# Kernel optimization log

Hardware: AMD Instinct MI355X
Metric: run time of the kernel (lower is better)

Reference implementation:

```python
import jax, jax.numpy as jnp
import numpy as np

L, KV, H, D, DM, F, V = 6, 1, 4, 256, 1152, 6912, 65536
HIST, T = 4095, 1
EPS = 1e-6


def setup_inputs():
    key = jax.random.key(0)
    ks = jax.random.split(key, 24)
    n = lambda k, s, sc=0.02: jax.random.normal(k, s, dtype=jnp.float32) * sc
    sf = D ** -0.25  # head_dim^-0.25 baked into q/k norm weights as in the source
    return {
        "input_ids": jax.random.randint(ks[0], (1, T), 0, V, dtype=jnp.int32),
        "attn_flag": 0,  # decode step: additive causal mask zeroed, as in the repo
        "key_cache": n(ks[1], (L, KV, D, HIST), 0.5),
        "value_cache": n(ks[2], (L, KV, HIST, D), 0.5),
        "embed_table": jax.random.randint(ks[3], (V, DM), 0, 256, dtype=jnp.int32),
        "embed_scale": jax.random.uniform(ks[4], (V, 1), minval=1e-4, maxval=1e-2, dtype=jnp.float32),
        "embed_zp": -jax.random.uniform(ks[5], (V, 1), minval=0.0, maxval=0.5, dtype=jnp.float32),
        "w_in_ln": 1.0 + n(ks[6], (L, DM)),
        "w_q_norm": (1.0 + n(ks[7], (L, D))) * sf,
        "w_k_norm": (1.0 + n(ks[8], (L, D))) * sf,
        "Wq": n(ks[9], (L, DM, H * D)),
        "Wk": n(ks[10], (L, DM, KV * D)),
        "Wv": n(ks[11], (L, DM, KV * D)),
        "Wo": n(ks[12], (L, H * D, DM)),
        "w_post_attn_ln": 1.0 + n(ks[13], (L, DM)),
        "w_pre_ffn_ln": 1.0 + n(ks[14], (L, DM)),
        "w_post_ffn_ln": 1.0 + n(ks[15], (L, DM)),
        "Wg": n(ks[16], (L, DM, F)),
        "Wu": n(ks[17], (L, DM, F)),
        "Wd": n(ks[18], (L, F, DM)),
        "w_final_norm": 1.0 + n(ks[19], (DM,)),
        "W_lm": n(ks[20], (DM, V)),
        "is_sliding": (jnp.arange(L) % 6) != 5,  # 5 local : 1 global pattern
    }


def _rms(x, w):
    return w * x / jnp.sqrt(jnp.mean(x * x, axis=-1, keepdims=True) + EPS)


def _rot_half(x, axis):
    x1, x2 = jnp.split(x, 2, axis=axis)
    return jnp.concatenate([-x2, x1], axis=axis)


def _rope(base, hist, S, d):
    pos = jnp.arange(hist, S, dtype=jnp.float32)[:, None]
    theta = base ** (-(jnp.arange(0, d, 2, dtype=jnp.float32) / d))
    ang = pos * theta
    c = jnp.concatenate([jnp.cos(ang)] * 2, axis=-1).astype(jnp.float16).astype(jnp.float32)
    s = jnp.concatenate([jnp.sin(ang)] * 2, axis=-1).astype(jnp.float16).astype(jnp.float32)
    return c, s  # (T, D), half-precision roundtrip mimics the .half() tables


def reference(input_ids, attn_flag, key_cache, value_cache, embed_table, embed_scale,
              embed_zp, w_in_ln, w_q_norm, w_k_norm, Wq, Wk, Wv, Wo, w_post_attn_ln,
              w_pre_ffn_ln, w_post_ffn_ln, Wg, Wu, Wd, w_final_norm, W_lm, is_sliding):
    Lc, KVc, Dd, hist = key_cache.shape
    Tq = input_ids.shape[1]
    S = hist + Tq
    Hh = Wq.shape[-1] // Dd
    G = Hh // KVc
    cos_g, sin_g = _rope(10000.0, hist, S, Dd)    # assigned to 'global' exactly as in source
    cos_l, sin_l = _rope(1000000.0, hist, S, Dd)  # assigned to 'local'
    mask = (jnp.arange(S)[None, :] > jnp.arange(Tq)[:, None]).astype(jnp.float32) * (-128.0 * float(attn_flag))  # (T,S)
    # int8-dequant embedding lookup: uint8 codes * per-row scale + per-row zero point
    h = embed_table[input_ids].astype(jnp.float32) * embed_scale[input_ids] + embed_zp[input_ids]  # (1,T,DM)

    def body(h, xs):
        ck, cv, slide, w_in, w_qn, w_kn, wq, wk, wv, wo, w_pa, w_pf, w_pof, wg, wu, wd = xs
        cq = jnp.where(slide, cos_l, cos_g)
        sq = jnp.where(slide, sin_l, sin_g)
        ckk, skk = cq.T, sq.T  # (D,T) for keys
        resid = h
        hn = _rms(h, w_in)                                                  # (1,T,DM)
        q = _rms((hn @ wq).reshape(Tq, Hh, Dd), w_qn).transpose(1, 0, 2)    # (H,T,D)
        k = _rms((hn @ wk).reshape(Tq, KVc, Dd), w_kn).transpose(1, 2, 0)   # (KV,D,T)
        v = (hn @ wv).reshape(Tq, KVc, Dd).transpose(1, 0, 2)               # (KV,T,D)
        q = q * cq + _rot_half(q, -1) * sq
        k = k * ckk[None] + _rot_half(k, 1) * skk[None]
        kf = jnp.concatenate([ck, k], axis=-1)   # (KV,D,S) new key cache
        vf = jnp.concatenate([cv, v], axis=1)    # (KV,S,D) new value cache
        kr = jnp.repeat(kf, G, axis=0)           # GQA repeat -> (H,D,S)
        vr = jnp.repeat(vf, G, axis=0)           # (H,S,D)
        attn = jax.nn.softmax(jnp.einsum('htd,hds->hts', q, kr) + mask[None], axis=-1)
        ao = jnp.einsum('hts,hsd->htd', attn, vr).transpose(1, 0, 2).reshape(1, Tq, Hh * Dd) @ wo
        h = resid + _rms(ao, w_pa)
        resid = h
        x = _rms(h, w_pf)
        m = (jax.nn.gelu(x @ wg, approximate=True) * (x @ wu)) @ wd
        h = resid + _rms(m, w_pof)
        return h, (kf, vf)

    h, (keys, values) = jax.lax.scan(
        body, h,
        (key_cache, value_cache, is_sliding, w_in_ln, w_q_norm, w_k_norm, Wq, Wk, Wv, Wo,
         w_post_attn_ln, w_pre_ffn_ln, w_post_ffn_ln, Wg, Wu, Wd))
    last = _rms(h[:, -1], w_final_norm)          # (1,DM)
    logits = last @ W_lm                          # (1,V)
    token = jnp.argmax(logits, axis=-1, keepdims=True).astype(jnp.int32)
    return keys, values, token
```

## Files before the change

kernel.cpp:

```cpp
#include <hip/hip_runtime.h>
#include <hip/hip_fp16.h>
#include <cmath>

#define LNUM 6
#define DM   1152
#define DHEAD 256
#define NH   4
#define FF   6912
#define VOC  65536
#define HIST 4095
#define SEQ  4096
#define EPSV 1e-6f

__device__ __forceinline__ float block_sum(float v, float* red4) {
#pragma unroll
    for (int off = 32; off; off >>= 1) v += __shfl_xor(v, off);
    int t = threadIdx.x;
    if ((t & 63) == 0) red4[t >> 6] = v;
    __syncthreads();
    float r = red4[0] + red4[1] + red4[2] + red4[3];
    __syncthreads();
    return r;
}

__global__ __launch_bounds__(256) void gk_copy(const float* __restrict__ kc,
                                               const float* __restrict__ vc,
                                               float* __restrict__ keys,
                                               float* __restrict__ vals) {
    int b = blockIdx.x;
    if (b < 24576) {
        int row = b >> 4;
        int s = ((b & 15) << 8) + threadIdx.x;
        if (s < HIST) keys[(size_t)row * SEQ + s] = kc[(size_t)row * HIST + s];
    } else {
        int r = (b - 24576) * 4 + (threadIdx.x >> 6);
        int d4 = threadIdx.x & 63;
        if (r < LNUM * HIST) {
            int l = r / HIST, sI = r - l * HIST;
            ((float4*)(vals + ((size_t)l * SEQ + sI) * DHEAD))[d4] =
                ((const float4*)(vc + (size_t)r * DHEAD))[d4];
        }
    }
}

__global__ __launch_bounds__(256) void gk_qkv(
    const float* __restrict__ Wq, const float* __restrict__ Wk, const float* __restrict__ Wv,
    const float* __restrict__ w_in, const float* __restrict__ w_pof_prev,
    const float* __restrict__ hprev, const float* __restrict__ dprev,
    const int* __restrict__ ids, const int* __restrict__ tbl,
    const float* __restrict__ escale, const float* __restrict__ ezp,
    float* __restrict__ hin_out, float* __restrict__ qkv_out, int has_prev) {
    __shared__ float xv[DM];
    __shared__ float red4[4];
    int t = threadIdx.x;
    if (has_prev) {
        float ss = 0.f;
        for (int i = t; i < DM; i += 256) { float d = dprev[i]; ss += d * d; }
        ss = block_sum(ss, red4);
        float inv = 1.f / sqrtf(ss / DM + EPSV);
        for (int i = t; i < DM; i += 256)
            xv[i] = hprev[i] + w_pof_prev[i] * dprev[i] * inv;
    } else {
        int tok = ids[0];
        float sc = escale[tok], z = ezp[tok];
        const int* row = tbl + (size_t)tok * DM;
        for (int i = t; i < DM; i += 256) xv[i] = (float)row[i] * sc + z;
    }
    __syncthreads();
    if (blockIdx.x == 0 && blockIdx.y == 0)
        for (int i = t; i < DM; i += 256) hin_out[i] = xv[i];
    float ss = 0.f;
    for (int i = t; i < DM; i += 256) { float v = xv[i]; ss += v * v; }
    ss = block_sum(ss, red4);
    float inv = 1.f / sqrtf(ss / DM + EPSV);
    for (int i = t; i < DM; i += 256) xv[i] = w_in[i] * xv[i] * inv;
    __syncthreads();

    int j = blockIdx.x * 256 + t;
    const float* W; int jj, ncol;
    if (j < 1024)      { W = Wq; jj = j;        ncol = 1024; }
    else if (j < 1280) { W = Wk; jj = j - 1024; ncol = 256; }
    else               { W = Wv; jj = j - 1280; ncol = 256; }
    int i0 = blockIdx.y * 36;
    float acc = 0.f;
#pragma unroll 4
    for (int ii = 0; ii < 36; ++ii)
        acc += xv[i0 + ii] * W[(size_t)(i0 + ii) * ncol + jj];
    atomicAdd(&qkv_out[j], acc);
}

__global__ __launch_bounds__(256) void gk_attn(
    const float* __restrict__ qkv, const float* __restrict__ w_qn,
    const float* __restrict__ w_kn, const int* __restrict__ attn_flag,
    float* __restrict__ keys_l, float* __restrict__ vals_l,
    float* __restrict__ po_part, float* __restrict__ sum_part, float rope_base) {
    __shared__ float lq[NH * DHEAD];
    __shared__ float lqf[NH * DHEAD];
    __shared__ float lkn[DHEAD];
    __shared__ float lkf[DHEAD];
    __shared__ float lv[DHEAD];
    __shared__ float lp[NH * 32];
    __shared__ float red4[4];
    int t = threadIdx.x;
    int s0 = blockIdx.x * 32;
    bool last = (blockIdx.x == gridDim.x - 1);

    int jm = t & 127;
    float theta = powf(rope_base, -(float)(2 * jm) / 256.f);
    float ang = 4095.f * theta;
    float c = __half2float(__float2half(cosf(ang)));
    float s = __half2float(__float2half(sinf(ang)));

    for (int h = 0; h < NH; ++h) lq[h * 256 + t] = qkv[h * 256 + t];
    lkn[t] = qkv[1024 + t];
    lv[t]  = qkv[1280 + t];
    __syncthreads();
    for (int h = 0; h < NH; ++h) {
        float v = lq[h * 256 + t];
        float ss = block_sum(v * v, red4);
        float inv = 1.f / sqrtf(ss / 256.f + EPSV);
        float qn = w_qn[t] * v * inv;
        lq[h * 256 + t] = qn;
        __syncthreads();
        float partner = (t < 128) ? -lq[h * 256 + t + 128] : lq[h * 256 + t - 128];
        lqf[h * 256 + t] = qn * c + partner * s;
    }
    {
        float v = lkn[t];
        float ss = block_sum(v * v, red4);
        float inv = 1.f / sqrtf(ss / 256.f + EPSV);
        float kn = w_kn[t] * v * inv;
        lkn[t] = kn;
        __syncthreads();
        float partner = (t < 128) ? -lkn[t + 128] : lkn[t - 128];
        lkf[t] = kn * c + partner * s;
    }
    __syncthreads();
    if (last) {
        keys_l[(size_t)t * SEQ + (SEQ - 1)] = lkf[t];
        vals_l[(size_t)(SEQ - 1) * DHEAD + t] = lv[t];
    }
    int sl = t & 31, dc = t >> 5;
    int sg = s0 + sl;
    bool self = last && (sl == 31);
    float a0 = 0, a1 = 0, a2 = 0, a3 = 0;
#pragma unroll 4
    for (int dd = 0; dd < 32; ++dd) {
        int d = dc * 32 + dd;
        float kv = self ? lkf[d] : keys_l[(size_t)d * SEQ + sg];
        a0 += lqf[0 * 256 + d] * kv;
        a1 += lqf[1 * 256 + d] * kv;
        a2 += lqf[2 * 256 + d] * kv;
        a3 += lqf[3 * 256 + d] * kv;
    }
    __syncthreads();
    lq[0 * 256 + t] = a0; lq[1 * 256 + t] = a1; lq[2 * 256 + t] = a2; lq[3 * 256 + t] = a3;
    __syncthreads();
    if (t < 32) {
        int af = attn_flag[0];
        float mk = (s0 + t > 0) ? -128.f * (float)af : 0.f;
        for (int h = 0; h < NH; ++h) {
            float sc_ = 0.f;
#pragma unroll
            for (int d8 = 0; d8 < 8; ++d8) sc_ += lq[h * 256 + d8 * 32 + t];
            lp[h * 32 + t] = expf(sc_ + mk);
        }
    }
    __syncthreads();
    if (t < NH) {
        float su = 0.f;
        for (int i = 0; i < 32; ++i) su += lp[t * 32 + i];
        sum_part[blockIdx.x * NH + t] = su;
    }
    float p0 = 0, p1 = 0, p2 = 0, p3 = 0;
#pragma unroll 4
    for (int ss_ = 0; ss_ < 32; ++ss_) {
        float v = (last && ss_ == 31) ? lv[t] : vals_l[(size_t)(s0 + ss_) * DHEAD + t];
        p0 += lp[0 * 32 + ss_] * v;
        p1 += lp[1 * 32 + ss_] * v;
        p2 += lp[2 * 32 + ss_] * v;
        p3 += lp[3 * 32 + ss_] * v;
    }
    float* po = po_part + (size_t)blockIdx.x * NH * DHEAD;
    po[0 * 256 + t] = p0; po[1 * 256 + t] = p1; po[2 * 256 + t] = p2; po[3 * 256 + t] = p3;
}

__global__ __launch_bounds__(256) void gk_wo(
    const float* __restrict__ po_part, const float* __restrict__ sum_part,
    const float* __restrict__ Wo_l, float* __restrict__ aproj) {
    __shared__ float x[64];
    __shared__ float hinv[NH];
    __shared__ float red4[4];
    int t = threadIdx.x;
    for (int h = 0; h < NH; ++h) {
        float v = (t < 128) ? sum_part[t * NH + h] : 0.f;
        float tot = block_sum(v, red4);
        if (t == 0) hinv[h] = 1.f / tot;
    }
    __syncthreads();
    int i0 = blockIdx.y * 64;
    if (t < 64) {
        float a = 0.f;
#pragma unroll 8
        for (int b = 0; b < 128; ++b) a += po_part[(size_t)b * 1024 + i0 + t];
        x[t] = a * hinv[(i0 + t) >> 8];
    }
    __syncthreads();
    int j = blockIdx.x * 256 + t;
    if (j < DM) {
        float acc = 0.f;
#pragma unroll 4
        for (int ii = 0; ii < 64; ++ii)
            acc += x[ii] * Wo_l[(size_t)(i0 + ii) * DM + j];
        atomicAdd(&aproj[j], acc);
    }
}

__global__ __launch_bounds__(256) void gk_gu(
    const float* __restrict__ Wg_l, const float* __restrict__ Wu_l,
    const float* __restrict__ w_pa, const float* __restrict__ w_pf,
    const float* __restrict__ hin, const float* __restrict__ aproj,
    float* __restrict__ hmid_out, float* __restrict__ gup) {
    __shared__ float xv[DM];
    __shared__ float red4[4];
    int t = threadIdx.x;
    float ss = 0.f;
    for (int i = t; i < DM; i += 256) { float a = aproj[i]; ss += a * a; }
    ss = block_sum(ss, red4);
    float inv = 1.f / sqrtf(ss / DM + EPSV);
    for (int i = t; i < DM; i += 256) xv[i] = hin[i] + w_pa[i] * aproj[i] * inv;
    __syncthreads();
    if (blockIdx.x == 0 && blockIdx.y == 0)
        for (int i = t; i < DM; i += 256) hmid_out[i] = xv[i];
    float s2 = 0.f;
    for (int i = t; i < DM; i += 256) { float v = xv[i]; s2 += v * v; }
    s2 = block_sum(s2, red4);
    float inv2 = 1.f / sqrtf(s2 / DM + EPSV);
    for (int i = t; i < DM; i += 256) xv[i] = w_pf[i] * xv[i] * inv2;
    __syncthreads();

    int j2 = blockIdx.x * 256 + t;
    const float2* W2; int jj2; float* dst;
    if (j2 < FF / 2) { W2 = (const float2*)Wg_l; jj2 = j2;
                       dst = gup + (size_t)blockIdx.y * 2 * FF + 2 * j2; }
    else             { W2 = (const float2*)Wu_l; jj2 = j2 - FF / 2;
                       dst = gup + (size_t)blockIdx.y * 2 * FF + FF + 2 * (j2 - FF / 2); }
    int i0 = blockIdx.y * 72;
    float ax = 0.f, ay = 0.f;
#pragma unroll 4
    for (int ii = 0; ii < 72; ++ii) {
        float xs = xv[i0 + ii];
        float2 w = W2[(size_t)(i0 + ii) * (FF / 2) + jj2];
        ax += xs * w.x; ay += xs * w.y;
    }
    dst[0] = ax; dst[1] = ay;
}

__global__ __launch_bounds__(256) void gk_wd(const float* __restrict__ gup,
                                             const float* __restrict__ Wd_l,
                                             float* __restrict__ dproj) {
    __shared__ float m[108];
    int t = threadIdx.x;
    int i0 = blockIdx.y * 108;
    if (t < 108) {
        float g = 0.f, u = 0.f;
#pragma unroll
        for (int p = 0; p < 16; ++p) {
            g += gup[(size_t)p * 2 * FF + i0 + t];
            u += gup[(size_t)p * 2 * FF + FF + i0 + t];
        }
        float gl = 0.5f * g * (1.f + tanhf(0.7978845608028654f * (g + 0.044715f * g * g * g)));
        m[t] = gl * u;
    }
    __syncthreads();
    int j = blockIdx.x * 256 + t;
    if (j < DM) {
        float acc = 0.f;
#pragma unroll 4
        for (int ii = 0; ii < 108; ++ii)
            acc += m[ii] * Wd_l[(size_t)(i0 + ii) * DM + j];
        atomicAdd(&dproj[j], acc);
    }
}

__global__ __launch_bounds__(256) void gk_logits(
    const float* __restrict__ W_lm, const float* __restrict__ w_pof5,
    const float* __restrict__ w_fin, const float* __restrict__ hmid5,
    const float* __restrict__ dproj5, float* __restrict__ lgp) {
    __shared__ float xv[DM];
    __shared__ float red4[4];
    int t = threadIdx.x;
    float ss = 0.f;
    for (int i = t; i < DM; i += 256) { float d = dproj5[i]; ss += d * d; }
    ss = block_sum(ss, red4);
    float inv = 1.f / sqrtf(ss / DM + EPSV);
    for (int i = t; i < DM; i += 256) xv[i] = hmid5[i] + w_pof5[i] * dproj5[i] * inv;
    __syncthreads();
    float s2 = 0.f;
    for (int i = t; i < DM; i += 256) { float v = xv[i]; s2 += v * v; }
    s2 = block_sum(s2, red4);
    float inv2 = 1.f / sqrtf(s2 / DM + EPSV);
    for (int i = t; i < DM; i += 256) xv[i] = w_fin[i] * xv[i] * inv2;
    __syncthreads();

    int j2 = blockIdx.x * 256 + t;
    int i0 = blockIdx.y * 192;
    const float2* W2 = (const float2*)W_lm;
    float ax = 0.f, ay = 0.f;
#pragma unroll 4
    for (int ii = 0; ii < 192; ++ii) {
        float xs = xv[i0 + ii];
        float2 w = W2[(size_t)(i0 + ii) * (VOC / 2) + j2];
        ax += xs * w.x; ay += xs * w.y;
    }
    float* dst = lgp + (size_t)blockIdx.y * VOC + 2 * j2;
    dst[0] = ax; dst[1] = ay;
}

__global__ __launch_bounds__(256) void gk_amax1(const float* __restrict__ lgp,
                                                float* __restrict__ pv, float* __restrict__ pi) {
    __shared__ float rv[256];
    __shared__ int ri[256];
    int t = threadIdx.x;
    int c1 = blockIdx.x * 512 + t, c2 = c1 + 256;
    float v1 = 0.f, v2 = 0.f;
#pragma unroll
    for (int p = 0; p < 6; ++p) {
        v1 += lgp[(size_t)p * VOC + c1];
        v2 += lgp[(size_t)p * VOC + c2];
    }
    float bv; int bi;
    if (v1 >= v2) { bv = v1; bi = c1; } else { bv = v2; bi = c2; }
    rv[t] = bv; ri[t] = bi; __syncthreads();
    for (int off = 128; off > 0; off >>= 1) {
        if (t < off) {
            float ov = rv[t + off]; int oi = ri[t + off];
            if (ov > rv[t] || (ov == rv[t] && oi < ri[t])) { rv[t] = ov; ri[t] = oi; }
        }
        __syncthreads();
    }
    if (t == 0) { pv[blockIdx.x] = rv[0]; pi[blockIdx.x] = (float)ri[0]; }
}

__global__ __launch_bounds__(128) void gk_amax2(const float* __restrict__ pv,
                                                const float* __restrict__ pi,
                                                float* __restrict__ tok_out) {
    __shared__ float rv[128];
    __shared__ int ri[128];
    int t = threadIdx.x;
    rv[t] = pv[t]; ri[t] = (int)pi[t]; __syncthreads();
    for (int off = 64; off > 0; off >>= 1) {
        if (t < off) {
            float ov = rv[t + off]; int oi = ri[t + off];
            if (ov > rv[t] || (ov == rv[t] && oi < ri[t])) { rv[t] = ov; ri[t] = oi; }
        }
        __syncthreads();
    }
    if (t == 0) tok_out[0] = (float)ri[0];
}

extern "C" void kernel_launch(void* const* d_in, const int* in_sizes, int n_in,
                              void* d_out, int out_size, void* d_ws, size_t ws_size,
                              hipStream_t stream) {
    const int*   input_ids   = (const int*)d_in[0];
    const int*   attn_flag   = (const int*)d_in[1];
    const float* key_cache   = (const float*)d_in[2];
    const float* value_cache = (const float*)d_in[3];
    const int*   embed_table = (const int*)d_in[4];
    const float* embed_scale = (const float*)d_in[5];
    const float* embed_zp    = (const float*)d_in[6];
    const float* w_in_ln     = (const float*)d_in[7];
    const float* w_q_norm    = (const float*)d_in[8];
    const float* w_k_norm    = (const float*)d_in[9];
    const float* Wq          = (const float*)d_in[10];
    const float* Wk          = (const float*)d_in[11];
    const float* Wv          = (const float*)d_in[12];
    const float* Wo          = (const float*)d_in[13];
    const float* w_pa        = (const float*)d_in[14];
    const float* w_pf        = (const float*)d_in[15];
    const float* w_pof       = (const float*)d_in[16];
    const float* Wg          = (const float*)d_in[17];
    const float* Wu          = (const float*)d_in[18];
    const float* Wd          = (const float*)d_in[19];
    const float* w_fin       = (const float*)d_in[20];
    const float* W_lm        = (const float*)d_in[21];

    float* keys = (float*)d_out;
    float* vals = keys + (size_t)LNUM * DHEAD * SEQ;
    float* tok_out = vals + (size_t)LNUM * SEQ * DHEAD;

    float* ws = (float*)d_ws;
    const size_t QKV_O = 0;
    const size_t AP_O  = QKV_O + (size_t)LNUM * 1536;
    const size_t DP_O  = AP_O + (size_t)LNUM * DM;
    const size_t ZEND  = DP_O + (size_t)LNUM * DM;
    const size_t POP_O = ZEND;
    const size_t SPS_O = POP_O + 128 * 1024;
    const size_t GUP_O = SPS_O + 128 * NH;
    const size_t LGP_O = GUP_O + (size_t)16 * 2 * FF;
    const size_t HIN_O = LGP_O + (size_t)6 * VOC;
    const size_t HM_O  = HIN_O + (size_t)LNUM * DM;
    const size_t AMV_O = HM_O + (size_t)LNUM * DM;
    const size_t AMI_O = AMV_O + 128;

    hipMemsetAsync(ws, 0, ZEND * sizeof(float), stream);
    gk_copy<<<24576 + 6144, 256, 0, stream>>>(key_cache, value_cache, keys, vals);

    for (int l = 0; l < LNUM; ++l) {
        float* QKVl = ws + QKV_O + (size_t)l * 1536;
        float* APl  = ws + AP_O + (size_t)l * DM;
        float* DPl  = ws + DP_O + (size_t)l * DM;
        float* HINl = ws + HIN_O + (size_t)l * DM;
        float* HMl  = ws + HM_O + (size_t)l * DM;
        float* keys_l = keys + (size_t)l * DHEAD * SEQ;
        float* vals_l = vals + (size_t)l * SEQ * DHEAD;

        gk_qkv<<<dim3(6, 32), 256, 0, stream>>>(
            Wq + (size_t)l * DM * 1024, Wk + (size_t)l * DM * 256,
            Wv + (size_t)l * DM * 256, w_in_ln + (size_t)l * DM,
            w_pof + (size_t)(l ? l - 1 : 0) * DM,
            (l ? ws + HM_O + (size_t)(l - 1) * DM : nullptr),
            (l ? ws + DP_O + (size_t)(l - 1) * DM : nullptr),
            input_ids, embed_table, embed_scale, embed_zp,
            HINl, QKVl, (l > 0) ? 1 : 0);

        gk_attn<<<128, 256, 0, stream>>>(
            QKVl, w_q_norm + (size_t)l * DHEAD, w_k_norm + (size_t)l * DHEAD,
            attn_flag, keys_l, vals_l, ws + POP_O, ws + SPS_O,
            ((l % 6) != 5) ? 1000000.0f : 10000.0f);

        gk_wo<<<dim3(5, 16), 256, 0, stream>>>(
            ws + POP_O, ws + SPS_O, Wo + (size_t)l * 1024 * DM, APl);

        gk_gu<<<dim3(27, 16), 256, 0, stream>>>(
            Wg + (size_t)l * DM * FF, Wu + (size_t)l * DM * FF,
            w_pa + (size_t)l * DM, w_pf + (size_t)l * DM, HINl, APl, HMl, ws + GUP_O);

        gk_wd<<<dim3(5, 64), 256, 0, stream>>>(ws + GUP_O, Wd + (size_t)l * FF * DM, DPl);
    }

    gk_logits<<<dim3(128, 6), 256, 0, stream>>>(
        W_lm, w_pof + (size_t)5 * DM, w_fin,
        ws + HM_O + (size_t)5 * DM, ws + DP_O + (size_t)5 * DM, ws + LGP_O);
    gk_amax1<<<128, 256, 0, stream>>>(ws + LGP_O, ws + AMV_O, ws + AMI_O);
    gk_amax2<<<1, 128, 0, stream>>>(ws + AMV_O, ws + AMI_O, tok_out);
}
```

Baseline: 596.0 us.

## Fuse per-layer decoder kernels into one persistent cooperative megakernel with grid syncs

Replaces the memset, cache copy and the five per-layer kernel launches with a single cooperative persistent kernel of 256 blocks that uses grid-wide syncs between stages. Work is redistributed into loops over work units, with new split-K tilings and in-block reductions before the atomics for Wo, gate/up and down projections. The goal is to remove launch overhead and inter-kernel gaps across roughly 30 launches. The risk is grid-sync cost, lower occupancy from 32KB of shared memory, and reduced parallelism on stages that now cover fewer units than before; a fallback multi-kernel path runs if the cooperative launch fails.

New measurement: 1.329 ms. 2.23x slower.

```diff
diff --git a/kernel.cpp b/kernel.cpp
--- a/kernel.cpp
+++ b/kernel.cpp
@@ -1,6 +1,9 @@
 #include <hip/hip_runtime.h>
 #include <hip/hip_fp16.h>
+#include <hip/hip_cooperative_groups.h>
 #include <cmath>
+
+namespace cg = cooperative_groups;
 
 #define LNUM 6
 #define DM   1152
@@ -11,8 +14,384 @@
 #define HIST 4095
 #define SEQ  4096
 #define EPSV 1e-6f
-
-__device__ __forceinline__ float block_sum(float v, float* red4) {
+#define NB   256
+
+#define QKV_O 0
+#define AP_O  9216
+#define DP_O  16128
+#define GU_O  23040
+#define ZEND  105984
+#define HIN_O 105984
+#define HM_O  112896
+#define POP_O 119808
+#define SPS_O 250880
+#define LGP_O 251392
+#define AMV_O 775680
+#define AMI_O 775936
+
+#define F_QKV_O 0
+#define F_AP_O  9216
+#define F_DP_O  16128
+#define F_ZEND  23040
+#define F_POP_O 23040
+#define F_SPS_O 154112
+#define F_GUP_O 154624
+#define F_LGP_O 375808
+#define F_HIN_O 769024
+#define F_HM_O  775936
+#define F_AMV_O 782848
+#define F_AMI_O 782976
+
+struct P {
+    const int* ids; const int* aflag;
+    const float* kc; const float* vc;
+    const int* tbl; const float* esc; const float* ezp;
+    const float* w_in; const float* w_qn; const float* w_kn;
+    const float* Wq; const float* Wk; const float* Wv; const float* Wo;
+    const float* w_pa; const float* w_pf; const float* w_pof;
+    const float* Wg; const float* Wu; const float* Wd;
+    const float* w_fin; const float* Wlm;
+    float* keys; float* vals; float* tok; float* ws;
+};
+
+__device__ __forceinline__ float bsum(float v, float* red4) {
+#pragma unroll
+    for (int off = 32; off; off >>= 1) v += __shfl_xor(v, off);
+    int t = threadIdx.x;
+    if ((t & 63) == 0) red4[t >> 6] = v;
+    __syncthreads();
+    float r = red4[0] + red4[1] + red4[2] + red4[3];
+    __syncthreads();
+    return r;
+}
+
+__global__ __launch_bounds__(256) void mega(P p) {
+    cg::grid_group gg = cg::this_grid();
+    __shared__ float sm[8192];
+    const int t = threadIdx.x, bid = blockIdx.x;
+    float* ws = p.ws;
+
+    {
+        for (int g = bid * 256 + t; g < ZEND; g += NB * 256) ws[g] = 0.f;
+        if (bid == 0) {
+            int tk = p.ids[0];
+            float sc = p.esc[tk], z = p.ezp[tk];
+            const int* row = p.tbl + (size_t)tk * DM;
+            for (int i = t; i < DM; i += 256) ws[HIN_O + i] = (float)row[i] * sc + z;
+        }
+        for (int rr = 0; rr < 6; ++rr) {
+            int row = bid * 6 + rr;
+            const float* src = p.kc + (size_t)row * HIST;
+            float* dst = p.keys + (size_t)row * SEQ;
+            for (int s = t; s < HIST; s += 256) dst[s] = src[s];
+        }
+        for (int rr = 0; rr < 24; ++rr) {
+            int r = bid * 96 + rr * 4 + (t >> 6);
+            if (r < LNUM * HIST) {
+                int l = r / HIST, sI = r - l * HIST;
+                ((float4*)(p.vals + ((size_t)l * SEQ + sI) * DHEAD))[t & 63] =
+                    ((const float4*)(p.vc + (size_t)r * DHEAD))[t & 63];
+            }
+        }
+    }
+    gg.sync();
+
+    for (int l = 0; l < LNUM; ++l) {
+        float* QKV = ws + QKV_O + l * 1536;
+        float* AP  = ws + AP_O + l * DM;
+        float* DP  = ws + DP_O + l * DM;
+        float* GU  = ws + GU_O + l * 13824;
+        float* HIN = ws + HIN_O + l * DM;
+        float* HM  = ws + HM_O + l * DM;
+        float* POP = ws + POP_O;
+        float* SPS = ws + SPS_O;
+        float* keys_l = p.keys + (size_t)l * DHEAD * SEQ;
+        float* vals_l = p.vals + (size_t)l * SEQ * DHEAD;
+
+        {
+            float* xv = sm; float* red4 = sm + 1280;
+            if (l == 0) {
+                for (int i = t; i < DM; i += 256) xv[i] = ws[HIN_O + i];
+                __syncthreads();
+            } else {
+                const float* hprev = ws + HM_O + (l - 1) * DM;
+                const float* dprev = ws + DP_O + (l - 1) * DM;
+                const float* wpof = p.w_pof + (l - 1) * DM;
+                float ss = 0.f;
+                for (int i = t; i < DM; i += 256) { float d = dprev[i]; ss += d * d; }
+                ss = bsum(ss, red4);
+                float inv = 1.f / sqrtf(ss / DM + EPSV);
+                for (int i = t; i < DM; i += 256)
+                    xv[i] = hprev[i] + wpof[i] * dprev[i] * inv;
+                __syncthreads();
+            }
+            if (bid == 0) for (int i = t; i < DM; i += 256) HIN[i] = xv[i];
+            float ss = 0.f;
+            for (int i = t; i < DM; i += 256) { float v = xv[i]; ss += v * v; }
+            ss = bsum(ss, red4);
+            float inv = 1.f / sqrtf(ss / DM + EPSV);
+            const float* w_in = p.w_in + l * DM;
+            for (int i = t; i < DM; i += 256) xv[i] = w_in[i] * xv[i] * inv;
+            __syncthreads();
+            for (int u = bid; u < 384; u += NB) {
+                int cgp = u % 6, kc = u / 6;
+                int j = cgp * 256 + t;
+                const float* W; int jj, ncol;
+                if (j < 1024)      { W = p.Wq + (size_t)l * DM * 1024; jj = j;        ncol = 1024; }
+                else if (j < 1280) { W = p.Wk + (size_t)l * DM * 256;  jj = j - 1024; ncol = 256; }
+                else               { W = p.Wv + (size_t)l * DM * 256;  jj = j - 1280; ncol = 256; }
+                int i0 = kc * 18;
+                float acc = 0.f;
+#pragma unroll
+                for (int ii = 0; ii < 18; ++ii)
+                    acc += xv[i0 + ii] * W[(size_t)(i0 + ii) * ncol + jj];
+                atomicAdd(&QKV[j], acc);
+            }
+        }
+        gg.sync();
+
+        if (bid < 128) {
+            float* lq = sm;
+            float* lqf = sm + 1024;
+            float* lkn = sm + 2048;
+            float* lkf = sm + 2304;
+            float* lv  = sm + 2560;
+            float* lp  = sm + 2816;
+            float* red4 = sm + 2944;
+            float* scred = sm + 3072;
+            float* pvred = sm + 4096;
+            int s0 = bid * 32;
+            bool lastb = (bid == 127);
+            float base = ((l % 6) != 5) ? 1000000.f : 10000.f;
+            int jm = t & 127;
+            float theta = powf(base, -(float)(2 * jm) / 256.f);
+            float ang = 4095.f * theta;
+            float c = __half2float(__float2half(cosf(ang)));
+            float s = __half2float(__float2half(sinf(ang)));
+            for (int h = 0; h < NH; ++h) lq[h * 256 + t] = QKV[h * 256 + t];
+            lkn[t] = QKV[1024 + t];
+            lv[t]  = QKV[1280 + t];
+            __syncthreads();
+            const float* wqn = p.w_qn + l * DHEAD;
+            const float* wkn = p.w_kn + l * DHEAD;
+            for (int h = 0; h < NH; ++h) {
+                float v = lq[h * 256 + t];
+                float ss = bsum(v * v, red4);
+                float inv = 1.f / sqrtf(ss / 256.f + EPSV);
+                float qn = wqn[t] * v * inv;
+                lq[h * 256 + t] = qn;
+                __syncthreads();
+                float partner = (t < 128) ? -lq[h * 256 + t + 128] : lq[h * 256 + t - 128];
+                lqf[h * 256 + t] = qn * c + partner * s;
+            }
+            {
+                float v = lkn[t];
+                float ss = bsum(v * v, red4);
+                float inv = 1.f / sqrtf(ss / 256.f + EPSV);
+                float kn = wkn[t] * v * inv;
+                lkn[t] = kn;
+                __syncthreads();
+                float partner = (t < 128) ? -lkn[t + 128] : lkn[t - 128];
+                lkf[t] = kn * c + partner * s;
+            }
+            __syncthreads();
+            if (lastb) {
+                keys_l[(size_t)t * SEQ + (SEQ - 1)] = lkf[t];
+                vals_l[(size_t)(SEQ - 1) * DHEAD + t] = lv[t];
+            }
+            int sl = t & 31, dc = t >> 5;
+            int sg = s0 + sl;
+            bool self = lastb && (sl == 31);
+            float a0 = 0, a1 = 0, a2 = 0, a3 = 0;
+#pragma unroll 4
+            for (int dd = 0; dd < 32; ++dd) {
+                int d = dc * 32 + dd;
+                float kv = self ? lkf[d] : keys_l[(size_t)d * SEQ + sg];
+                a0 += lqf[d] * kv; a1 += lqf[256 + d] * kv;
+                a2 += lqf[512 + d] * kv; a3 += lqf[768 + d] * kv;
+            }
+            scred[dc * 128 + sl]      = a0;
+            scred[dc * 128 + 32 + sl] = a1;
+            scred[dc * 128 + 64 + sl] = a2;
+            scred[dc * 128 + 96 + sl] = a3;
+            __syncthreads();
+            if (t < 32) {
+                int af = p.aflag[0];
+                float mk = (s0 + t > 0) ? -128.f * (float)af : 0.f;
+                for (int h = 0; h < NH; ++h) {
+                    float sc_ = 0.f;
+#pragma unroll
+                    for (int d8 = 0; d8 < 8; ++d8) sc_ += scred[d8 * 128 + h * 32 + t];
+                    lp[h * 32 + t] = expf(sc_ + mk);
+                }
+            }
+            __syncthreads();
+            if (t < NH) {
+                float su = 0.f;
+                for (int i = 0; i < 32; ++i) su += lp[t * 32 + i];
+                SPS[bid * NH + t] = su;
+            }
+            int d4 = t & 63, sr = t >> 6;
+            float4 ac0 = {0,0,0,0}, ac1 = {0,0,0,0}, ac2 = {0,0,0,0}, ac3 = {0,0,0,0};
+#pragma unroll
+            for (int ss_ = 0; ss_ < 8; ++ss_) {
+                int sI = sr * 8 + ss_;
+                float4 v;
+                if (lastb && sI == 31) v = ((float4*)lv)[d4];
+                else v = ((const float4*)(vals_l + (size_t)(s0 + sI) * DHEAD))[d4];
+                float p0 = lp[sI], p1 = lp[32 + sI], p2 = lp[64 + sI], p3 = lp[96 + sI];
+                ac0.x += p0 * v.x; ac0.y += p0 * v.y; ac0.z += p0 * v.z; ac0.w += p0 * v.w;
+                ac1.x += p1 * v.x; ac1.y += p1 * v.y; ac1.z += p1 * v.z; ac1.w += p1 * v.w;
+                ac2.x += p2 * v.x; ac2.y += p2 * v.y; ac2.z += p2 * v.z; ac2.w += p2 * v.w;
+                ac3.x += p3 * v.x; ac3.y += p3 * v.y; ac3.z += p3 * v.z; ac3.w += p3 * v.w;
+            }
+            ((float4*)(pvred + sr * 1024 + 0))[d4]   = ac0;
+            ((float4*)(pvred + sr * 1024 + 256))[d4] = ac1;
+            ((float4*)(pvred + sr * 1024 + 512))[d4] = ac2;
+            ((float4*)(pvred + sr * 1024 + 768))[d4] = ac3;
+            __syncthreads();
+            for (int o = t; o < 1024; o += 256) {
+                float v = pvred[o] + pvred[1024 + o] + pvred[2048 + o] + pvred[3072 + o];
+                POP[(size_t)bid * 1024 + o] = v;
+            }
+        }
+        gg.sync();
+
+        {
+            float* hinv = sm;
+            float* xred = sm + 8;
+            float* xl = sm + 272;
+            float* red4 = sm + 312;
+            float* wored = sm + 320;
+            for (int h = 0; h < NH; ++h) {
+                float v = (t < 128) ? SPS[t * NH + h] : 0.f;
+                float tot = bsum(v, red4);
+                if (t == 0) hinv[h] = 1.f / tot;
+            }
+            __syncthreads();
+            const float* Wo_l = p.Wo + (size_t)l * 1024 * DM;
+            for (int u = bid; u < 288; u += NB) {
+                __syncthreads();
+                int cgp = u % 9, kc = u / 9;
+                int i0 = kc * 32;
+                { int li = t & 31, bg = t >> 5;
+                  float a = 0.f;
+                  for (int b = bg * 16; b < bg * 16 + 16; ++b) a += POP[(size_t)b * 1024 + i0 + li];
+                  xred[bg * 32 + li] = a; }
+                __syncthreads();
+                if (t < 32) {
+                    float a = 0.f;
+#pragma unroll
+                    for (int bg = 0; bg < 8; ++bg) a += xred[bg * 32 + t];
+                    xl[t] = a * hinv[(i0 + t) >> 8];
+                }
+                __syncthreads();
+                int col = cgp * 128 + (t & 127);
+                int kh = t >> 7;
+                float acc = 0.f;
+#pragma unroll
+                for (int r = 0; r < 16; ++r) {
+                    int li = kh * 16 + r;
+                    acc += xl[li] * Wo_l[(size_t)(i0 + li) * DM + col];
+                }
+                wored[t] = acc;
+                __syncthreads();
+                if (t < 128) atomicAdd(&AP[cgp * 128 + t], wored[t] + wored[128 + t]);
+            }
+        }
+        gg.sync();
+
+        {
+            float* xv = sm; float* red4 = sm + 1152; float* gred = sm + 1184;
+            float ss = 0.f;
+            for (int i = t; i < DM; i += 256) { float a = AP[i]; ss += a * a; }
+            ss = bsum(ss, red4);
+            float inv = 1.f / sqrtf(ss / DM + EPSV);
+            const float* wpa = p.w_pa + l * DM;
+            for (int i = t; i < DM; i += 256) xv[i] = HIN[i] + wpa[i] * AP[i] * inv;
+            __syncthreads();
+            if (bid == 0) for (int i = t; i < DM; i += 256) HM[i] = xv[i];
+            float s2 = 0.f;
+            for (int i = t; i < DM; i += 256) { float v = xv[i]; s2 += v * v; }
+            s2 = bsum(s2, red4);
+            float inv2 = 1.f / sqrtf(s2 / DM + EPSV);
+            const float* wpf = p.w_pf + l * DM;
+            for (int i = t; i < DM; i += 256) xv[i] = wpf[i] * xv[i] * inv2;
+            __syncthreads();
+            for (int u = bid; u < 486; u += NB) {
+                __syncthreads();
+                int cgi = u % 54, kc = u / 54;
+                bool isU = cgi >= 27;
+                int cgp = isU ? cgi - 27 : cgi;
+                const float* W = (isU ? p.Wu : p.Wg) + (size_t)l * DM * FF;
+                int f4c = t & 63, ks = t >> 6;
+                int colf = cgp * 64 + f4c;
+                int i0 = kc * 128 + ks * 32;
+                float4 acc = {0,0,0,0};
+#pragma unroll 4
+                for (int r = 0; r < 32; ++r) {
+                    float xs = xv[i0 + r];
+                    float4 w = ((const float4*)(W + (size_t)(i0 + r) * FF))[colf];
+                    acc.x += xs * w.x; acc.y += xs * w.y; acc.z += xs * w.z; acc.w += xs * w.w;
+                }
+                ((float4*)gred)[ks * 64 + f4c] = acc;
+                __syncthreads();
+                if (ks == 0) {
+                    float4 r0 = ((float4*)gred)[f4c],       r1 = ((float4*)gred)[64 + f4c],
+                           r2 = ((float4*)gred)[128 + f4c], r3 = ((float4*)gred)[192 + f4c];
+                    float* dst = GU + (isU ? FF : 0) + colf * 4;
+                    atomicAdd(dst + 0, r0.x + r1.x + r2.x + r3.x);
+                    atomicAdd(dst + 1, r0.y + r1.y + r2.y + r3.y);
+                    atomicAdd(dst + 2, r0.z + r1.z + r2.z + r3.z);
+                    atomicAdd(dst + 3, r0.w + r1.w + r2.w + r3.w);
+                }
+            }
+        }
+        gg.sync();
+
+        {
+            float* m = sm;
+            float* wred = sm + 128;
+            const float* Wd_l = p.Wd + (size_t)l * FF * DM;
+            for (int u = bid; u < 486; u += NB) {
+                __syncthreads();
+                int cgp = u % 9, kc = u / 9;
+                int i0 = kc * 128;
+                if (t < 128) {
+                    float g = GU[i0 + t], uu = GU[FF + i0 + t];
+                    float gl = 0.5f * g * (1.f + tanhf(0.7978845608028654f * (g + 0.044715f * g * g * g)));
+                    m[t] = gl * uu;
+                }
+                __syncthreads();
+                int f4c = t & 31, ks = t >> 5;
+                float4 acc = {0,0,0,0};
+#pragma unroll 4
+                for (int r = 0; r < 16; ++r) {
+                    int li = ks * 16 + r;
+                    float xs = m[li];
+                    float4 w = ((const float4*)(Wd_l + (size_t)(i0 + li) * DM))[cgp * 32 + f4c];
+                    acc.x += xs * w.x; acc.y += xs * w.y; acc.z += xs * w.z; acc.w += xs * w.w;
+                }
+                ((float4*)wred)[ks * 32 + f4c] = acc;
+                __syncthreads();
+                if (ks == 0) {
+                    float sx = 0, sy = 0, sz = 0, sw = 0;
+#pragma unroll
+                    for (int k2 = 0; k2 < 8; ++k2) {
+                        float4 r = ((float4*)wred)[k2 * 32 + f4c];
+                        sx += r.x; sy += r.y; sz += r.z; sw += r.w;
+                    }
+                    float* dst = DP + cgp * 128 + f4c * 4;
+                    atomicAdd(dst + 0, sx); atomicAdd(dst + 1, sy);
+                    atomicAdd(dst + 2, sz); atomicAdd(dst + 3, sw);
+                }
+            }
+        }
+        gg.sync();
+    }
+}
+
+__device__ __forceinline__ float block_sum256(float v, float* red4) {
 #pragma unroll
     for (int off = 32; off; off >>= 1) v += __shfl_xor(v, off);
     int t = threadIdx.x;
@@ -56,7 +435,7 @@
     if (has_prev) {
         float ss = 0.f;
         for (int i = t; i < DM; i += 256) { float d = dprev[i]; ss += d * d; }
-        ss = block_sum(ss, red4);
+        ss = block_sum256(ss, red4);
         float inv = 1.f / sqrtf(ss / DM + EPSV);
         for (int i = t; i < DM; i += 256)
             xv[i] = hprev[i] + w_pof_prev[i] * dprev[i] * inv;
@@ -71,7 +450,7 @@
         for (int i = t; i < DM; i += 256) hin_out[i] = xv[i];
     float ss = 0.f;
     for (int i = t; i < DM; i += 256) { float v = xv[i]; ss += v * v; }
-    ss = block_sum(ss, red4);
+    ss = block_sum256(ss, red4);
     float inv = 1.f / sqrtf(ss / DM + EPSV);
     for (int i = t; i < DM; i += 256) xv[i] = w_in[i] * xv[i] * inv;
     __syncthreads();
@@ -117,7 +496,7 @@
     __syncthreads();
     for (int h = 0; h < NH; ++h) {
         float v = lq[h * 256 + t];
-        float ss = block_sum(v * v, red4);
+        float ss = block_sum256(v * v, red4);
         float inv = 1.f / sqrtf(ss / 256.f + EPSV);
         float qn = w_qn[t] * v * inv;
         lq[h * 256 + t] = qn;
@@ -127,7 +506,7 @@
     }
     {
         float v = lkn[t];
-        float ss = block_sum(v * v, red4);
+        float ss = block_sum256(v * v, red4);
         float inv = 1.f / sqrtf(ss / 256.f + EPSV);
         float kn = w_kn[t] * v * inv;
         lkn[t] = kn;
@@ -194,7 +573,7 @@
     int t = threadIdx.x;
     for (int h = 0; h < NH; ++h) {
         float v = (t < 128) ? sum_part[t * NH + h] : 0.f;
-        float tot = block_sum(v, red4);
+        float tot = block_sum256(v, red4);
         if (t == 0) hinv[h] = 1.f / tot;
     }
     __syncthreads();
@@ -226,7 +605,7 @@
     int t = threadIdx.x;
     float ss = 0.f;
     for (int i = t; i < DM; i += 256) { float a = aproj[i]; ss += a * a; }
-    ss = block_sum(ss, red4);
+    ss = block_sum256(ss, red4);
     float inv = 1.f / sqrtf(ss / DM + EPSV);
     for (int i = t; i < DM; i += 256) xv[i] = hin[i] + w_pa[i] * aproj[i] * inv;
     __syncthreads();
@@ -234,7 +613,7 @@
         for (int i = t; i < DM; i += 256) hmid_out[i] = xv[i];
     float s2 = 0.f;
     for (int i = t; i < DM; i += 256) { float v = xv[i]; s2 += v * v; }
-    s2 = block_sum(s2, red4);
+    s2 = block_sum256(s2, red4);
     float inv2 = 1.f / sqrtf(s2 / DM + EPSV);
     for (int i = t; i < DM; i += 256) xv[i] = w_pf[i] * xv[i] * inv2;
     __syncthreads();
@@ -292,13 +671,13 @@
     int t = threadIdx.x;
     float ss = 0.f;
     for (int i = t; i < DM; i += 256) { float d = dproj5[i]; ss += d * d; }
-    ss = block_sum(ss, red4);
+    ss = block_sum256(ss, red4);
     float inv = 1.f / sqrtf(ss / DM + EPSV);
     for (int i = t; i < DM; i += 256) xv[i] = hmid5[i] + w_pof5[i] * dproj5[i] * inv;
     __syncthreads();
     float s2 = 0.f;
     for (int i = t; i < DM; i += 256) { float v = xv[i]; s2 += v * v; }
-    s2 = block_sum(s2, red4);
+    s2 = block_sum256(s2, red4);
     float inv2 = 1.f / sqrtf(s2 / DM + EPSV);
     for (int i = t; i < DM; i += 256) xv[i] = w_fin[i] * xv[i] * inv2;
     __syncthreads();
@@ -362,86 +741,83 @@
 extern "C" void kernel_launch(void* const* d_in, const int* in_sizes, int n_in,
                               void* d_out, int out_size, void* d_ws, size_t ws_size,
                               hipStream_t stream) {
-    const int*   input_ids   = (const int*)d_in[0];
-    const int*   attn_flag   = (const int*)d_in[1];
-    const float* key_cache   = (const float*)d_in[2];
-    const float* value_cache = (const float*)d_in[3];
-    const int*   embed_table = (const int*)d_in[4];
-    const float* embed_scale = (const float*)d_in[5];
-    const float* embed_zp    = (const float*)d_in[6];
-    const float* w_in_ln     = (const float*)d_in[7];
-    const float* w_q_norm    = (const float*)d_in[8];
-    const float* w_k_norm    = (const float*)d_in[9];
-    const float* Wq          = (const float*)d_in[10];
-    const float* Wk          = (const float*)d_in[11];
-    const float* Wv          = (const float*)d_in[12];
-    const float* Wo          = (const float*)d_in[13];
-    const float* w_pa        = (const float*)d_in[14];
-    const float* w_pf        = (const float*)d_in[15];
-    const float* w_pof       = (const float*)d_in[16];
-    const float* Wg          = (const float*)d_in[17];
-    const float* Wu          = (const float*)d_in[18];
-    const float* Wd          = (const float*)d_in[19];
-    const float* w_fin       = (const float*)d_in[20];
-    const float* W_lm        = (const float*)d_in[21];
-
-    float* keys = (float*)d_out;
-    float* vals = keys + (size_t)LNUM * DHEAD * SEQ;
-    float* tok_out = vals + (size_t)LNUM * SEQ * DHEAD;
-
+    P p;
+    p.ids   = (const int*)d_in[0];
+    p.aflag = (const int*)d_in[1];
+    p.kc    = (const float*)d_in[2];
+    p.vc    = (const float*)d_in[3];
+    p.tbl   = (const int*)d_in[4];
+    p.esc   = (const float*)d_in[5];
+    p.ezp   = (const float*)d_in[6];
+    p.w_in  = (const float*)d_in[7];
+    p.w_qn  = (const float*)d_in[8];
+    p.w_kn  = (const float*)d_in[9];
+    p.Wq    = (const float*)d_in[10];
+    p.Wk    = (const float*)d_in[11];
+    p.Wv    = (const float*)d_in[12];
+    p.Wo    = (const float*)d_in[13];
+    p.w_pa  = (const float*)d_in[14];
+    p.w_pf  = (const float*)d_in[15];
+    p.w_pof = (const float*)d_in[16];
+    p.Wg    = (const float*)d_in[17];
+    p.Wu    = (const float*)d_in[18];
+    p.Wd    = (const float*)d_in[19];
+    p.w_fin = (const float*)d_in[20];
+    p.Wlm   = (const float*)d_in[21];
+    p.keys  = (float*)d_out;
+    p.vals  = p.keys + (size_t)LNUM * DHEAD * SEQ;
+    p.tok   = p.vals + (size_t)LNUM * SEQ * DHEAD;
+    p.ws    = (float*)d_ws;
     float* ws = (float*)d_ws;
-    const size_t QKV_O = 0;
-    const size_t AP_O  = QKV_O + (size_t)LNUM * 1536;
-    const size_t DP_O  = AP_O + (size_t)LNUM * DM;
-    const size_t ZEND  = DP_O + (size_t)LNUM * DM;
-    const size_t POP_O = ZEND;
-    const size_t SPS_O = POP_O + 128 * 1024;
-    const size_t GUP_O = SPS_O + 128 * NH;
-    const size_t LGP_O = GUP_O + (size_t)16 * 2 * FF;
-    const size_t HIN_O = LGP_O + (size_t)6 * VOC;
-    const size_t HM_O  = HIN_O + (size_t)LNUM * DM;
-    const size_t AMV_O = HM_O + (size_t)LNUM * DM;
-    const size_t AMI_O = AMV_O + 128;
-
-    hipMemsetAsync(ws, 0, ZEND * sizeof(float), stream);
-    gk_copy<<<24576 + 6144, 256, 0, stream>>>(key_cache, value_cache, keys, vals);
-
-    for (int l = 0; l < LNUM; ++l) {
-        float* QKVl = ws + QKV_O + (size_t)l * 1536;
-        float* APl  = ws + AP_O + (size_t)l * DM;
-        float* DPl  = ws + DP_O + (size_t)l * DM;
-        float* HINl = ws + HIN_O + (size_t)l * DM;
-        float* HMl  = ws + HM_O + (size_t)l * DM;
-        float* keys_l = keys + (size_t)l * DHEAD * SEQ;
-        float* vals_l = vals + (size_t)l * SEQ * DHEAD;
-
-        gk_qkv<<<dim3(6, 32), 256, 0, stream>>>(
-            Wq + (size_t)l * DM * 1024, Wk + (size_t)l * DM * 256,
-            Wv + (size_t)l * DM * 256, w_in_ln + (size_t)l * DM,
-            w_pof + (size_t)(l ? l - 1 : 0) * DM,
-            (l ? ws + HM_O + (size_t)(l - 1) * DM : nullptr),
-            (l ? ws + DP_O + (size_t)(l - 1) * DM : nullptr),
-            input_ids, embed_table, embed_scale, embed_zp,
-            HINl, QKVl, (l > 0) ? 1 : 0);
-
-        gk_attn<<<128, 256, 0, stream>>>(
-            QKVl, w_q_norm + (size_t)l * DHEAD, w_k_norm + (size_t)l * DHEAD,
-            attn_flag, keys_l, vals_l, ws + POP_O, ws + SPS_O,
-            ((l % 6) != 5) ? 1000000.0f : 10000.0f);
-
-        gk_wo<<<dim3(5, 16), 256, 0, stream>>>(
-            ws + POP_O, ws + SPS_O, Wo + (size_t)l * 1024 * DM, APl);
-
-        gk_gu<<<dim3(27, 16), 256, 0, stream>>>(
-            Wg + (size_t)l * DM * FF, Wu + (size_t)l * DM * FF,
-            w_pa + (size_t)l * DM, w_pf + (size_t)l * DM, HINl, APl, HMl, ws + GUP_O);
-
-        gk_wd<<<dim3(5, 64), 256, 0, stream>>>(ws + GUP_O, Wd + (size_t)l * FF * DM, DPl);
-    }
-
-    gk_logits<<<dim3(128, 6), 256, 0, stream>>>(
-        W_lm, w_pof + (size_t)5 * DM, w_fin,
-        ws + HM_O + (size_t)5 * DM, ws + DP_O + (size_t)5 * DM, ws + LGP_O);
-    gk_amax1<<<128, 256, 0, stream>>>(ws + LGP_O, ws + AMV_O, ws + AMI_O);
-    gk_amax2<<<1, 128, 0, stream>>>(ws + AMV_O, ws + AMI_O, tok_out);
-}
+
+    void* args[] = { &p };
+    hipError_t err = hipLaunchCooperativeKernel((void*)mega, dim3(NB), dim3(256), args, 0, stream);
+
+    if (err == hipSuccess) {
+        gk_logits<<<dim3(128, 6), 256, 0, stream>>>(
+            p.Wlm, p.w_pof + (size_t)5 * DM, p.w_fin,
+            ws + HM_O + (size_t)5 * DM, ws + DP_O + (size_t)5 * DM, ws + LGP_O);
+        gk_amax1<<<128, 256, 0, stream>>>(ws + LGP_O, ws + AMV_O, ws + AMI_O);
+        gk_amax2<<<1, 128, 0, stream>>>(ws + AMV_O, ws + AMI_O, p.tok);
+    } else {
+        hipMemsetAsync(ws, 0, F_ZEND * sizeof(float), stream);
+        gk_copy<<<24576 + 6144, 256, 0, stream>>>(p.kc, p.vc, p.keys, p.vals);
+        for (int l = 0; l < LNUM; ++l) {
+            float* QKVl = ws + F_QKV_O + (size_t)l * 1536;
+            float* APl  = ws + F_AP_O + (size_t)l * DM;
+            float* DPl  = ws + F_DP_O + (size_t)l * DM;
+            float* HINl = ws + F_HIN_O + (size_t)l * DM;
+            float* HMl  = ws + F_HM_O + (size_t)l * DM;
+            float* keys_l = p.keys + (size_t)l * DHEAD * SEQ;
+            float* vals_l = p.vals + (size_t)l * SEQ * DHEAD;
+
+            gk_qkv<<<dim3(6, 32), 256, 0, stream>>>(
+                p.Wq + (size_t)l * DM * 1024, p.Wk + (size_t)l * DM * 256,
+                p.Wv + (size_t)l * DM * 256, p.w_in + (size_t)l * DM,
+                p.w_pof + (size_t)(l ? l - 1 : 0) * DM,
+                (l ? ws + F_HM_O + (size_t)(l - 1) * DM : nullptr),
+                (l ? ws + F_DP_O + (size_t)(l - 1) * DM : nullptr),
+                p.ids, p.tbl, p.esc, p.ezp,
+                HINl, QKVl, (l > 0) ? 1 : 0);
+
+            gk_attn<<<128, 256, 0, stream>>>(
+                QKVl, p.w_qn + (size_t)l * DHEAD, p.w_kn + (size_t)l * DHEAD,
+                p.aflag, keys_l, vals_l, ws + F_POP_O, ws + F_SPS_O,
+                ((l % 6) != 5) ? 1000000.0f : 10000.0f);
+
+            gk_wo<<<dim3(5, 16), 256, 0, stream>>>(
+                ws + F_POP_O, ws + F_SPS_O, p.Wo + (size_t)l * 1024 * DM, APl);
+
+            gk_gu<<<dim3(27, 16), 256, 0, stream>>>(
+                p.Wg + (size_t)l * DM * FF, p.Wu + (size_t)l * DM * FF,
+                p.w_pa + (size_t)l * DM, p.w_pf + (size_t)l * DM, HINl, APl, HMl, ws + F_GUP_O);
+
+            gk_wd<<<dim3(5, 64), 256, 0, stream>>>(ws + F_GUP_O, p.Wd + (size_t)l * FF * DM, DPl);
+        }
+        gk_logits<<<dim3(128, 6), 256, 0, stream>>>(
+            p.Wlm, p.w_pof + (size_t)5 * DM, p.w_fin,
+            ws + F_HM_O + (size_t)5 * DM, ws + F_DP_O + (size_t)5 * DM, ws + F_LGP_O);
+        gk_amax1<<<128, 256, 0, stream>>>(ws + F_LGP_O, ws + F_AMV_O, ws + F_AMI_O);
+        gk_amax2<<<1, 128, 0, stream>>>(ws + F_AMV_O, ws + F_AMI_O, p.tok);
+    }
+}
```
